# Optimization experiments

Measured on AMD Instinct MI355X. Metric: run time of the kernel, lower is better.

Reference implementation:

```python
import jax, jax.numpy as jnp
import numpy as np

NUM_HEADS = 8
LN_EPS = 1e-5


def layer_norm_chw(x, w, b):
    # LayerNorm over (C, H, W) jointly, elementwise affine of shape (C, H, W)
    mu = jnp.mean(x, axis=(1, 2, 3), keepdims=True)
    var = jnp.mean(jnp.square(x - mu), axis=(1, 2, 3), keepdims=True)
    return (x - mu) * jax.lax.rsqrt(var + LN_EPS) * w[None] + b[None]


def conv1x1(x, w, b):
    # 1x1 conv == per-pixel matmul. x: (B,C,H,W), w: (O,C), b: (O,)
    return jnp.einsum('bcxy,oc->boxy', x, w) + b[None, :, None, None]


def setup_inputs() -> dict:
    key = jax.random.key(0)
    ks = jax.random.split(key, 8)
    B, C, H, W = 16, 512, 64, 64
    Dq, Dv, Dh = 512, 512, 2048
    s = lambda fan_in: 1.0 / np.sqrt(fan_in)
    return {
        'x': jax.random.normal(ks[0], (B, C, H, W), jnp.float32),
        'ln1_w': jnp.ones((C, H, W), jnp.float32),
        'ln1_b': jnp.zeros((C, H, W), jnp.float32),
        'q_w': jax.random.normal(ks[1], (Dq, C), jnp.float32) * s(C),
        'q_b': jnp.zeros((Dq,), jnp.float32),
        'k_w': jax.random.normal(ks[2], (Dq, C), jnp.float32) * s(C),
        'k_b': jnp.zeros((Dq,), jnp.float32),
        'v_w': jax.random.normal(ks[3], (Dv, C), jnp.float32) * s(C),
        'v_b': jnp.zeros((Dv,), jnp.float32),
        'hu_w': jax.random.normal(ks[4], (C, Dv), jnp.float32) * s(Dv),
        'hu_b': jnp.zeros((C,), jnp.float32),
        'ln2_w': jnp.ones((C, H, W), jnp.float32),
        'ln2_b': jnp.zeros((C, H, W), jnp.float32),
        'ff1_w': jax.random.normal(ks[5], (Dh, C), jnp.float32) * s(C),
        'ff1_b': jnp.zeros((Dh,), jnp.float32),
        'ff2_w': jax.random.normal(ks[6], (C, Dh), jnp.float32) * s(Dh),
        'ff2_b': jnp.zeros((C,), jnp.float32),
    }


def reference(x, ln1_w, ln1_b, q_w, q_b, k_w, k_b, v_w, v_b,
              hu_w, hu_b, ln2_w, ln2_b, ff1_w, ff1_b, ff2_w, ff2_b):
    B, C, H, W = x.shape
    h = NUM_HEADS

    a = layer_norm_chw(x, ln1_w, ln1_b)
    Q = conv1x1(a, q_w, q_b)   # (B, Dq, H, W)
    K = conv1x1(a, k_w, k_b)   # (B, Dq, H, W)
    V = conv1x1(a, v_w, v_b)   # (B, Dv, H, W)

    Dq, Dv = Q.shape[1], V.shape[1]
    # softmax over channel dim for Q (per pixel, over all Dq channels)
    Q = jax.nn.softmax(Q, axis=1)
    # softmax over flattened spatial dim for K (per channel)
    K = jax.nn.softmax(K.reshape(B, Dq, H * W), axis=-1).reshape(B, Dq, H, W)

    # split heads: (B, h, d, H, W)
    Qh = Q.reshape(B, h, Dq // h, H, W)
    Kh = K.reshape(B, h, Dq // h, H, W)
    Vh = V.reshape(B, h, Dv // h, H, W)

    # linear attention: KV = sum_xy K ⊗ V, then per-pixel KV^T @ Q
    KV = jnp.einsum('bhkxy,bhvxy->bhkv', Kh, Vh)        # (B, h, dq, dv)
    attn = jnp.einsum('bhkv,bhkxy->bhvxy', KV, Qh)      # (B, h, dv, H, W)
    attn = attn.reshape(B, Dv, H, W)
    attn = conv1x1(attn, hu_w, hu_b)                    # (B, C, H, W)

    x = x + attn
    x = layer_norm_chw(x, ln2_w, ln2_b)
    ff = conv1x1(jax.nn.gelu(conv1x1(x, ff1_w, ff1_b), approximate=False), ff2_w, ff2_b)
    return x + ff
```

## Files before the change

### kernel.cpp

```cpp
#include <hip/hip_runtime.h>
#include <math.h>

#define BATCH 16
#define CCH   512
#define HWS   4096
#define CHW   (CCH*HWS)
#define DHFF  2048
#define NHEAD 8
#define HD    64
#define QKVLD 1536
#define LNEPS 1e-5f

typedef unsigned short u16;
typedef __bf16 bf16x8 __attribute__((ext_vector_type(8)));
typedef float f32x4 __attribute__((ext_vector_type(4)));

__device__ __forceinline__ float gelu_f(float x) {
    float y = 1.5957691216057308f * x * (1.0f + 0.044715f * x * x);
    return x / (1.0f + __expf(-y));
}
__device__ __forceinline__ u16 f2bf(float f) {
    union { float f; unsigned u; } c; c.f = f;
    unsigned r = c.u + 0x7FFFu + ((c.u >> 16) & 1u);
    return (u16)(r >> 16);
}
__device__ __forceinline__ float bf2f(u16 h) {
    union { unsigned u; float f; } c; c.u = ((unsigned)h) << 16; return c.f;
}
__device__ __forceinline__ uint2 pack_bf16x4(float v0, float v1, float v2, float v3) {
    union { uint2 u; __bf16 b[4]; } o;
    o.b[0] = (__bf16)v0; o.b[1] = (__bf16)v1; o.b[2] = (__bf16)v2; o.b[3] = (__bf16)v3;
    return o.u;
}
__device__ __forceinline__ void gld16(const u16* g, u16* l) {
    __builtin_amdgcn_global_load_lds((const __attribute__((address_space(1))) unsigned*)g,
                                     (__attribute__((address_space(3))) unsigned*)l, 16, 0, 0);
}

template<int K>
__device__ __forceinline__ void gemm_core(const u16* __restrict__ A,
                                          const u16* __restrict__ B,
                                          int m0, int n0,
                                          u16 (&As)[2][128 * 32],
                                          u16 (&Bs)[2][128 * 32],
                                          f32x4 (&acc)[4][4]) {
    const int tid = threadIdx.x;
    const int lane = tid & 63;
    const int w = tid >> 6;
    const int wm = (w & 1) * 64, wn = (w >> 1) * 64;
    const int ls = lane & 15, lq = lane >> 4;
#pragma unroll
    for (int i = 0; i < 4; ++i)
#pragma unroll
        for (int j = 0; j < 4; ++j) acc[i][j] = (f32x4){0.f, 0.f, 0.f, 0.f};

    const int srow = w * 16 + (lane >> 2);
    const int scol = (lane & 3) * 8;
    const u16* gA0 = A + (size_t)(m0 + srow) * K + scol;
    const u16* gA1 = gA0 + (size_t)64 * K;
    const u16* gB0 = B + (size_t)(n0 + srow) * K + scol;
    const u16* gB1 = gB0 + (size_t)64 * K;
    const int lo = w * 512;

    gld16(gA0, &As[0][lo]);
    gld16(gA1, &As[0][2048 + lo]);
    gld16(gB0, &Bs[0][lo]);
    gld16(gB1, &Bs[0][2048 + lo]);
    __syncthreads();

#pragma unroll 8
    for (int kt = 0; kt < K; kt += 32) {
        const int cur = (kt >> 5) & 1;
        const int nx = cur ^ 1;
        if (kt + 32 < K) {
            gld16(gA0 + kt + 32, &As[nx][lo]);
            gld16(gA1 + kt + 32, &As[nx][2048 + lo]);
            gld16(gB0 + kt + 32, &Bs[nx][lo]);
            gld16(gB1 + kt + 32, &Bs[nx][2048 + lo]);
        }
        bf16x8 af[4], bfv[4];
#pragma unroll
        for (int i = 0; i < 4; ++i)
            af[i] = *(bf16x8*)&As[cur][(wm + i * 16 + ls) * 32 + lq * 8];
#pragma unroll
        for (int j = 0; j < 4; ++j)
            bfv[j] = *(bf16x8*)&Bs[cur][(wn + j * 16 + ls) * 32 + lq * 8];
#pragma unroll
        for (int i = 0; i < 4; ++i)
#pragma unroll
            for (int j = 0; j < 4; ++j)
                acc[i][j] = __builtin_amdgcn_mfma_f32_16x16x32_bf16(bfv[j], af[i], acc[i][j], 0, 0, 0);
        if (kt + 32 < K)
            __syncthreads();
    }
}

__global__ __launch_bounds__(256) void stats_k(const float* __restrict__ src,
                                               float* __restrict__ st) {
    int b = blockIdx.y;
    const float4* p = (const float4*)(src + (size_t)b * CHW + (size_t)blockIdx.x * (CHW / 64));
    float s = 0.f, ss = 0.f;
    for (int i = threadIdx.x; i < (CHW / 64 / 4); i += 256) {
        float4 v = p[i];
        s  += v.x + v.y + v.z + v.w;
        ss += v.x * v.x + v.y * v.y + v.z * v.z + v.w * v.w;
    }
    __shared__ float r1[256], r2[256];
    int t = threadIdx.x;
    r1[t] = s; r2[t] = ss; __syncthreads();
    for (int o = 128; o > 0; o >>= 1) {
        if (t < o) { r1[t] += r1[t + o]; r2[t] += r2[t + o]; }
        __syncthreads();
    }
    if (t == 0) { atomicAdd(&st[2 * b], r1[0]); atomicAdd(&st[2 * b + 1], r2[0]); }
}

__global__ __launch_bounds__(256) void cvt_k(const float* __restrict__ src,
                                             u16* __restrict__ dst, int n4) {
    int i = blockIdx.x * 256 + threadIdx.x;
    if (i >= n4) return;
    float4 v = ((const float4*)src)[i];
    ((uint2*)dst)[i] = pack_bf16x4(v.x, v.y, v.z, v.w);
}

__global__ __launch_bounds__(256) void tr_k(const float* __restrict__ src,
                                            float* __restrict__ dst) {
    int p0 = blockIdx.x * 32, c0 = blockIdx.y * 32;
    __shared__ float T[32][33];
    int tx = threadIdx.x & 31, ty = threadIdx.x >> 5;
#pragma unroll
    for (int i = 0; i < 4; ++i)
        T[ty + i * 8][tx] = src[(size_t)(c0 + ty + i * 8) * HWS + p0 + tx];
    __syncthreads();
#pragma unroll
    for (int i = 0; i < 4; ++i)
        dst[(size_t)(p0 + ty + i * 8) * CCH + c0 + tx] = T[tx][ty + i * 8];
}

__global__ __launch_bounds__(256) void ln1t_k(const float* __restrict__ x,
                                              const float* __restrict__ w,
                                              const float* __restrict__ bb,
                                              const float* __restrict__ st,
                                              u16* __restrict__ a, int cb) {
    int p0 = blockIdx.x * 32, c0 = blockIdx.y * 32, bl = blockIdx.z;
    int b = cb + bl;
    float mean = st[2 * b] * (1.0f / CHW);
    float var  = st[2 * b + 1] * (1.0f / CHW) - mean * mean;
    float rstd = rsqrtf(var + LNEPS);
    __shared__ float T[32][33];
    int tx = threadIdx.x & 31, ty = threadIdx.x >> 5;
    const float* xb = x + (size_t)b * CHW;
#pragma unroll
    for (int i = 0; i < 4; ++i) {
        size_t o = (size_t)(c0 + ty + i * 8) * HWS + p0 + tx;
        T[ty + i * 8][tx] = (xb[o] - mean) * rstd * w[o] + bb[o];
    }
    __syncthreads();
    u16* ab = a + (size_t)bl * CHW;
#pragma unroll
    for (int i = 0; i < 4; ++i)
        ab[(size_t)(p0 + ty + i * 8) * CCH + c0 + tx] = f2bf(T[tx][ty + i * 8]);
}

template<int K, int ACT>
__global__ __launch_bounds__(256) void gemm_tn(const u16* __restrict__ A,
                                               const u16* __restrict__ B,
                                               const float* __restrict__ bias,
                                               u16* __restrict__ Out,
                                               int ldo, int nt) {
    __shared__ u16 As[2][128 * 32];
    __shared__ u16 Bs[2][128 * 32];
    const int cpx = gridDim.x >> 3;
    const int wg = ((int)blockIdx.x & 7) * cpx + ((int)blockIdx.x >> 3);
    const int m0 = (wg / nt) * 128;
    const int n0 = (wg % nt) * 128;
    f32x4 acc[4][4];
    gemm_core<K>(A, B, m0, n0, As, Bs, acc);

    const int lane = threadIdx.x & 63;
    const int w = threadIdx.x >> 6;
    const int wm = (w & 1) * 64, wn = (w >> 1) * 64;
    const int ls = lane & 15, lq = lane >> 4;
#pragma unroll
    for (int j = 0; j < 4; ++j) {
        int nb = n0 + wn + j * 16 + lq * 4;
        float4 bv = *(const float4*)&bias[nb];
#pragma unroll
        for (int i = 0; i < 4; ++i) {
            int m = m0 + wm + i * 16 + ls;
            float v0 = acc[i][j][0] + bv.x;
            float v1 = acc[i][j][1] + bv.y;
            float v2 = acc[i][j][2] + bv.z;
            float v3 = acc[i][j][3] + bv.w;
            if (ACT) { v0 = gelu_f(v0); v1 = gelu_f(v1); v2 = gelu_f(v2); v3 = gelu_f(v3); }
            *(uint2*)(Out + (size_t)m * ldo + nb) = pack_bf16x4(v0, v1, v2, v3);
        }
    }
}

__global__ __launch_bounds__(256) void gemm_hu_resid(const u16* __restrict__ A,
                                                     const u16* __restrict__ B,
                                                     const float* __restrict__ bias,
                                                     float* __restrict__ r,
                                                     const float* __restrict__ x,
                                                     float* __restrict__ pstat, int cb) {
    __shared__ u16 As[2][128 * 32];
    __shared__ u16 Bs[2][128 * 32];
    __shared__ float r1[256], r2[256];
    const int nt = 4;
    const int cpx = gridDim.x >> 3;
    const int wg = ((int)blockIdx.x & 7) * cpx + ((int)blockIdx.x >> 3);
    const int m0 = (wg / nt) * 128;
    const int n0 = (wg % nt) * 128;
    f32x4 acc[4][4];
    gemm_core<512>(A, B, m0, n0, As, Bs, acc);

    const int lane = threadIdx.x & 63;
    const int w = threadIdx.x >> 6;
    const int wm = (w & 1) * 64, wn = (w >> 1) * 64;
    const int ls = lane & 15, lq = lane >> 4;
    const int bl = m0 >> 12;
    const int p0loc = m0 & 4095;
    const float* xb = x + (size_t)(cb + bl) * CHW;
    float* rb = r + (size_t)bl * CHW;
    float s = 0.f, ss = 0.f;
#pragma unroll
    for (int j = 0; j < 4; ++j) {
        int nb = n0 + wn + j * 16 + lq * 4;
        float4 bv = *(const float4*)&bias[nb];
#pragma unroll
        for (int i = 0; i < 4; ++i) {
            int p = p0loc + wm + i * 16 + ls;
            float v0 = acc[i][j][0] + bv.x + xb[(size_t)(nb + 0) * HWS + p];
            float v1 = acc[i][j][1] + bv.y + xb[(size_t)(nb + 1) * HWS + p];
            float v2 = acc[i][j][2] + bv.z + xb[(size_t)(nb + 2) * HWS + p];
            float v3 = acc[i][j][3] + bv.w + xb[(size_t)(nb + 3) * HWS + p];
            *(float4*)(rb + (size_t)p * CCH + nb) = (float4){v0, v1, v2, v3};
            s  += v0 + v1 + v2 + v3;
            ss += v0 * v0 + v1 * v1 + v2 * v2 + v3 * v3;
        }
    }
    int t = threadIdx.x;
    __syncthreads();
    r1[t] = s; r2[t] = ss; __syncthreads();
    for (int o = 128; o > 0; o >>= 1) {
        if (t < o) { r1[t] += r1[t + o]; r2[t] += r2[t + o]; }
        __syncthreads();
    }
    if (t == 0) {
        int slot = ((p0loc >> 7) << 2) + (wg % nt);
        float* pp = pstat + ((size_t)(cb + bl) * 128 + slot) * 2;
        pp[0] = r1[0]; pp[1] = r2[0];
    }
}

__global__ __launch_bounds__(256) void gemm_ff2_final(const u16* __restrict__ A,
                                                      const u16* __restrict__ B,
                                                      const float* __restrict__ bias,
                                                      float* __restrict__ out,
                                                      const u16* __restrict__ x2,
                                                      int cb) {
    __shared__ union {
        struct { u16 As[2][128 * 32]; u16 Bs[2][128 * 32]; } g;
        float Tt[64][130];
    } shm;
    const int nt = 4;
    const int cpx = gridDim.x >> 3;
    const int wg = ((int)blockIdx.x & 7) * cpx + ((int)blockIdx.x >> 3);
    const int m0 = (wg / nt) * 128;
    const int n0 = (wg % nt) * 128;
    f32x4 acc[4][4];
    gemm_core<2048>(A, B, m0, n0, shm.g.As, shm.g.Bs, acc);

    const int tid = threadIdx.x;
    const int lane = tid & 63;
    const int w = tid >> 6;
    const int wm = (w & 1) * 64, wn = (w >> 1) * 64;
    const int ls = lane & 15, lq = lane >> 4;
    const int bl = m0 >> 12;
    const int p0loc = m0 & 4095;
    const u16* x2b = x2 + (size_t)bl * CHW;
    float* ob = out + (size_t)(cb + bl) * CHW;

    const int row = tid >> 2, mc = (tid & 3) * 32;
#pragma unroll
    for (int rnd = 0; rnd < 2; ++rnd) {
        __syncthreads();
        if ((wn >> 6) == rnd) {
#pragma unroll
            for (int j = 0; j < 4; ++j) {
                int nloc = wn + j * 16 + lq * 4;
                float4 bv = *(const float4*)&bias[n0 + nloc];
#pragma unroll
                for (int i = 0; i < 4; ++i) {
                    int m = wm + i * 16 + ls;
                    uint2 xr = *(const uint2*)&x2b[(size_t)(p0loc + m) * CCH + n0 + nloc];
                    u16* xp = (u16*)&xr;
                    int tr = nloc & 63;
                    shm.Tt[tr + 0][m] = acc[i][j][0] + bv.x + bf2f(xp[0]);
                    shm.Tt[tr + 1][m] = acc[i][j][1] + bv.y + bf2f(xp[1]);
                    shm.Tt[tr + 2][m] = acc[i][j][2] + bv.z + bf2f(xp[2]);
                    shm.Tt[tr + 3][m] = acc[i][j][3] + bv.w + bf2f(xp[3]);
                }
            }
        }
        __syncthreads();
        float* orow = ob + (size_t)(n0 + rnd * 64 + row) * HWS + p0loc + mc;
#pragma unroll
        for (int q = 0; q < 32; q += 4)
            *(float4*)(orow + q) = *(float4*)&shm.Tt[row][mc + q];
    }
}

__global__ __launch_bounds__(256) void softmax_row_k(u16* __restrict__ QKV) {
    int m = blockIdx.x * 4 + (threadIdx.x >> 6);
    int lane = threadIdx.x & 63;
    u16* row = QKV + (size_t)m * QKVLD + lane * 8;
    uint4 raw = *(uint4*)row;
    u16* pr = (u16*)&raw;
    float v[8];
#pragma unroll
    for (int i = 0; i < 8; ++i) v[i] = bf2f(pr[i]);
    float mx = v[0];
#pragma unroll
    for (int i = 1; i < 8; ++i) mx = fmaxf(mx, v[i]);
    for (int o = 32; o > 0; o >>= 1) mx = fmaxf(mx, __shfl_xor(mx, o, 64));
    float s = 0.f;
#pragma unroll
    for (int i = 0; i < 8; ++i) { v[i] = __expf(v[i] - mx); s += v[i]; }
    for (int o = 32; o > 0; o >>= 1) s += __shfl_xor(s, o, 64);
    float inv = 1.0f / s;
#pragma unroll
    for (int i = 0; i < 8; ++i) pr[i] = f2bf(v[i] * inv);
    *(uint4*)row = raw;
}

__global__ __launch_bounds__(256) void kcolstat_k(const u16* __restrict__ QKV,
                                                  float* __restrict__ kpart) {
    int pc = blockIdx.x, bl = blockIdx.y;
    int cg = threadIdx.x & 63;
    int ps = threadIdx.x >> 6;
    const u16* base = QKV + (size_t)bl * HWS * QKVLD + CCH + cg * 8;
    int p0 = pc * 256 + ps * 64;
    float m[8];
#pragma unroll
    for (int i = 0; i < 8; ++i) m[i] = -1e30f;
    for (int p = p0; p < p0 + 64; ++p) {
        uint4 r = *(const uint4*)(base + (size_t)p * QKVLD);
        u16* rp = (u16*)&r;
#pragma unroll
        for (int i = 0; i < 8; ++i) m[i] = fmaxf(m[i], bf2f(rp[i]));
    }
    __shared__ float red[4][512];
#pragma unroll
    for (int i = 0; i < 8; ++i) red[ps][cg * 8 + i] = m[i];
    __syncthreads();
#pragma unroll
    for (int i = 0; i < 8; ++i)
        m[i] = fmaxf(fmaxf(red[0][cg * 8 + i], red[1][cg * 8 + i]),
                     fmaxf(red[2][cg * 8 + i], red[3][cg * 8 + i]));
    __syncthreads();
    float s[8];
#pragma unroll
    for (int i = 0; i < 8; ++i) s[i] = 0.f;
    for (int p = p0; p < p0 + 64; ++p) {
        uint4 r = *(const uint4*)(base + (size_t)p * QKVLD);
        u16* rp = (u16*)&r;
#pragma unroll
        for (int i = 0; i < 8; ++i) s[i] += __expf(bf2f(rp[i]) - m[i]);
    }
#pragma unroll
    for (int i = 0; i < 8; ++i) red[ps][cg * 8 + i] = s[i];
    __syncthreads();
    if (ps == 0) {
        float* outp = kpart + (((size_t)bl * 16 + pc) * 512 + cg * 8) * 2;
#pragma unroll
        for (int i = 0; i < 8; ++i) {
            float sv = red[0][cg * 8 + i] + red[1][cg * 8 + i] +
                       red[2][cg * 8 + i] + red[3][cg * 8 + i];
            outp[2 * i] = m[i]; outp[2 * i + 1] = sv;
        }
    }
}

__global__ __launch_bounds__(256) void kcolmerge_k(const float* __restrict__ kpart,
                                                   float* __restrict__ kstat) {
    int bl = blockIdx.x;
#pragma unroll
    for (int j = 0; j < 2; ++j) {
        int col = threadIdx.x * 2 + j;
        float m = -1e30f;
        for (int pc = 0; pc < 16; ++pc)
            m = fmaxf(m, kpart[(((size_t)bl * 16 + pc) * 512 + col) * 2]);
        float s = 0.f;
        for (int pc = 0; pc < 16; ++pc) {
            const float* p = kpart + (((size_t)bl * 16 + pc) * 512 + col) * 2;
            s += p[1] * __expf(p[0] - m);
        }
        kstat[((size_t)bl * 512 + col) * 2]     = m;
        kstat[((size_t)bl * 512 + col) * 2 + 1] = 1.0f / s;
    }
}

__global__ __launch_bounds__(256) void kv_k2(const u16* __restrict__ QKV,
                                             const float* __restrict__ kstat,
                                             float* __restrict__ KV) {
    int pc = blockIdx.x, h = blockIdx.y, bl = blockIdx.z;
    const u16* kbase = QKV + (size_t)bl * HWS * QKVLD + CCH + h * HD;
    const u16* vbase = kbase + CCH;
    float* kvb = KV + ((size_t)bl * NHEAD + h) * (HD * HD);
    __shared__ float Ks[64][65], Vs[64][65];
    __shared__ float Ms[64], Is[64];
    int tid = threadIdx.x;
    if (tid < 64) {
        const float* sp = kstat + ((size_t)bl * 512 + h * HD + tid) * 2;
        Ms[tid] = sp[0]; Is[tid] = sp[1];
    }
    int tk = tid >> 4, tv = tid & 15;
    float acc[4][4];
#pragma unroll
    for (int i = 0; i < 4; ++i)
#pragma unroll
        for (int j = 0; j < 4; ++j) acc[i][j] = 0.f;

    for (int s = 0; s < 4; ++s) {
        int pbase = pc * 256 + s * 64;
        __syncthreads();
#pragma unroll
        for (int j = 0; j < 2; ++j) {
            int li = tid + j * 256;
            int pl = li >> 3, c8 = (li & 7) * 8;
            uint4 kr = *(const uint4*)(kbase + (size_t)(pbase + pl) * QKVLD + c8);
            uint4 vr = *(const uint4*)(vbase + (size_t)(pbase + pl) * QKVLD + c8);
            u16* kp = (u16*)&kr; u16* vp = (u16*)&vr;
#pragma unroll
            for (int t = 0; t < 8; ++t) {
                Ks[pl][c8 + t] = __expf(bf2f(kp[t]) - Ms[c8 + t]) * Is[c8 + t];
                Vs[pl][c8 + t] = bf2f(vp[t]);
            }
        }
        __syncthreads();
#pragma unroll 4
        for (int p = 0; p < 64; ++p) {
            float ka[4], va[4];
#pragma unroll
            for (int i = 0; i < 4; ++i) { ka[i] = Ks[p][tk * 4 + i]; va[i] = Vs[p][tv * 4 + i]; }
#pragma unroll
            for (int i = 0; i < 4; ++i)
#pragma unroll
                for (int j = 0; j < 4; ++j) acc[i][j] += ka[i] * va[j];
        }
    }
#pragma unroll
    for (int i = 0; i < 4; ++i)
#pragma unroll
        for (int j = 0; j < 4; ++j)
            atomicAdd(&kvb[(size_t)(tk * 4 + i) * HD + tv * 4 + j], acc[i][j]);
}

__global__ __launch_bounds__(256) void attn_k2(const u16* __restrict__ QKV,
                                               const float* __restrict__ KV,
                                               u16* __restrict__ attnRaw) {
    int pt = blockIdx.x, h = blockIdx.y, bl = blockIdx.z;
    const u16* qbase = QKV + (size_t)bl * HWS * QKVLD + h * HD;
    const float* kvb = KV + ((size_t)bl * NHEAD + h) * (HD * HD);
    __shared__ float KVs[64][68], Qs[64][68];
    int tid = threadIdx.x;
#pragma unroll
    for (int j = 0; j < 4; ++j) {
        int li = tid + j * 256;
        int k = li >> 4, c4 = (li & 15) * 4;
        *(float4*)&KVs[k][c4] = *(const float4*)(kvb + (size_t)k * HD + c4);
    }
#pragma unroll
    for (int j = 0; j < 2; ++j) {
        int li = tid + j * 256;
        int pl = li >> 3, c8 = (li & 7) * 8;
        uint4 qr = *(const uint4*)(qbase + (size_t)(pt * 64 + pl) * QKVLD + c8);
        u16* qp = (u16*)&qr;
#pragma unroll
        for (int t = 0; t < 8; ++t) Qs[pl][c8 + t] = bf2f(qp[t]);
    }
    __syncthreads();
    int tp = tid >> 4, tv = tid & 15;
    float acc[4][4];
#pragma unroll
    for (int i = 0; i < 4; ++i)
#pragma unroll
        for (int j = 0; j < 4; ++j) acc[i][j] = 0.f;
#pragma unroll 4
    for (int k = 0; k < 64; ++k) {
        float qa[4], kv4[4];
#pragma unroll
        for (int i = 0; i < 4; ++i) { qa[i] = Qs[tp * 4 + i][k]; kv4[i] = KVs[k][tv * 4 + i]; }
#pragma unroll
        for (int i = 0; i < 4; ++i)
#pragma unroll
            for (int j = 0; j < 4; ++j) acc[i][j] += qa[i] * kv4[j];
    }
#pragma unroll
    for (int i = 0; i < 4; ++i) {
        *(uint2*)(attnRaw + (size_t)(bl * HWS + pt * 64 + tp * 4 + i) * CCH + h * HD + tv * 4) =
            pack_bf16x4(acc[i][0], acc[i][1], acc[i][2], acc[i][3]);
    }
}

__global__ __launch_bounds__(128) void red2_k(const float* __restrict__ pstat,
                                              float* __restrict__ st, int cb) {
    int b = cb + blockIdx.x;
    const float* p = pstat + (size_t)b * 256;
    int t = threadIdx.x;
    float s = p[2 * t], ss = p[2 * t + 1];
    for (int o = 32; o > 0; o >>= 1) { s += __shfl_down(s, o, 64); ss += __shfl_down(ss, o, 64); }
    __shared__ float sh[4];
    if ((t & 63) == 0) { sh[(t >> 6) * 2] = s; sh[(t >> 6) * 2 + 1] = ss; }
    __syncthreads();
    if (t == 0) { st[32 + 2 * b] = sh[0] + sh[2]; st[32 + 2 * b + 1] = sh[1] + sh[3]; }
}

__global__ __launch_bounds__(256) void ln2a_k(const float* __restrict__ r,
                                              const float* __restrict__ w2t,
                                              const float* __restrict__ b2t,
                                              const float* __restrict__ st,
                                              u16* __restrict__ x2, int cb) {
    size_t i4 = (size_t)blockIdx.x * 256 + threadIdx.x;
    int bl = (int)(i4 / (CHW / 4));
    int b = cb + bl;
    size_t off4 = i4 % (CHW / 4);
    float mean = st[32 + 2 * b] * (1.0f / CHW);
    float var  = st[32 + 2 * b + 1] * (1.0f / CHW) - mean * mean;
    float rstd = rsqrtf(var + LNEPS);
    float4 v  = ((const float4*)(r + (size_t)bl * CHW))[off4];
    float4 wv = ((const float4*)w2t)[off4];
    float4 bv = ((const float4*)b2t)[off4];
    ((uint2*)(x2 + (size_t)bl * CHW))[off4] =
        pack_bf16x4((v.x - mean) * rstd * wv.x + bv.x,
                    (v.y - mean) * rstd * wv.y + bv.y,
                    (v.z - mean) * rstd * wv.z + bv.z,
                    (v.w - mean) * rstd * wv.w + bv.w);
}

extern "C" void kernel_launch(void* const* d_in, const int* in_sizes, int n_in,
                              void* d_out, int out_size, void* d_ws, size_t ws_size,
                              hipStream_t stream) {
    const float* x    = (const float*)d_in[0];
    const float* ln1w = (const float*)d_in[1];
    const float* ln1b = (const float*)d_in[2];
    const float* qw   = (const float*)d_in[3];
    const float* qb   = (const float*)d_in[4];
    const float* kw   = (const float*)d_in[5];
    const float* kb   = (const float*)d_in[6];
    const float* vw   = (const float*)d_in[7];
    const float* vb   = (const float*)d_in[8];
    const float* huw  = (const float*)d_in[9];
    const float* hub  = (const float*)d_in[10];
    const float* ln2w = (const float*)d_in[11];
    const float* ln2b = (const float*)d_in[12];
    const float* f1w  = (const float*)d_in[13];
    const float* f1b  = (const float*)d_in[14];
    const float* f2w  = (const float*)d_in[15];
    const float* f2b  = (const float*)d_in[16];
    float* out = (float*)d_out;
    float* ws = (float*)d_ws;

    float* stats = ws;
    float* qkvb  = ws + 64;
    u16*   wqkv  = (u16*)(ws + 1600);
    u16*   whu   = (u16*)(ws + 394816);
    u16*   wf1   = (u16*)(ws + 525888);
    u16*   wf2   = (u16*)(ws + 1050176);
    float* w2t   = ws + 1574464;
    float* b2t   = ws + 3671616;
    float* pstat = ws + 5768768;
    float* kpart = ws + 5834304;
    float* kstat = ws + 6096448;
    float* kvbuf = ws + 6112832;

    int G = 16;
    while (G > 1 && (6112832ull + (size_t)G * 5275648ull) * 4ull > ws_size) G >>= 1;
    const int nch = BATCH / G;
    const size_t U = (size_t)G * CHW;

    float* R       = kvbuf + (size_t)G * 32768;
    u16*   a_bf    = (u16*)R;
    u16*   QKVb    = (u16*)(R + U / 2);
    float* rbuf    = R + 3 * U / 2;
    u16*   x2bf    = (u16*)R;
    u16*   Hbuf    = (u16*)(R + U / 2);

    hipMemsetAsync(stats, 0, 64 * sizeof(float), stream);

    cvt_k<<<dim3(256), 256, 0, stream>>>(qw, wqkv, 65536);
    cvt_k<<<dim3(256), 256, 0, stream>>>(kw, wqkv + 262144, 65536);
    cvt_k<<<dim3(256), 256, 0, stream>>>(vw, wqkv + 524288, 65536);
    cvt_k<<<dim3(256), 256, 0, stream>>>(huw, whu, 65536);
    cvt_k<<<dim3(1024), 256, 0, stream>>>(f1w, wf1, 262144);
    cvt_k<<<dim3(1024), 256, 0, stream>>>(f2w, wf2, 262144);
    tr_k<<<dim3(128, 16), 256, 0, stream>>>(ln2w, w2t);
    tr_k<<<dim3(128, 16), 256, 0, stream>>>(ln2b, b2t);
    hipMemcpyAsync(qkvb,        qb, 512 * sizeof(float), hipMemcpyDeviceToDevice, stream);
    hipMemcpyAsync(qkvb + 512,  kb, 512 * sizeof(float), hipMemcpyDeviceToDevice, stream);
    hipMemcpyAsync(qkvb + 1024, vb, 512 * sizeof(float), hipMemcpyDeviceToDevice, stream);

    stats_k<<<dim3(64, BATCH), 256, 0, stream>>>(x, stats);

    for (int g = 0; g < nch; ++g) {
        const int cb = g * G;
        const int mt = G * 32;
        ln1t_k<<<dim3(128, 16, G), 256, 0, stream>>>(x, ln1w, ln1b, stats, a_bf, cb);
        gemm_tn<512, 0><<<dim3(mt * 12), 256, 0, stream>>>(a_bf, wqkv, qkvb, QKVb, QKVLD, 12);
        softmax_row_k<<<dim3(G * 1024), 256, 0, stream>>>(QKVb);
        kcolstat_k<<<dim3(16, G), 256, 0, stream>>>(QKVb, kpart);
        kcolmerge_k<<<dim3(G), 256, 0, stream>>>(kpart, kstat);
        hipMemsetAsync(kvbuf, 0, (size_t)G * 32768 * sizeof(float), stream);
        kv_k2<<<dim3(16, NHEAD, G), 256, 0, stream>>>(QKVb, kstat, kvbuf);
        attn_k2<<<dim3(64, NHEAD, G), 256, 0, stream>>>(QKVb, kvbuf, a_bf);
        gemm_hu_resid<<<dim3(mt * 4), 256, 0, stream>>>(a_bf, whu, hub, rbuf, x, pstat, cb);
        red2_k<<<dim3(G), 128, 0, stream>>>(pstat, stats, cb);
        ln2a_k<<<dim3(G * 2048), 256, 0, stream>>>(rbuf, w2t, b2t, stats, x2bf, cb);
        gemm_tn<512, 1><<<dim3(mt * 16), 256, 0, stream>>>(x2bf, wf1, f1b, Hbuf, DHFF, 16);
        gemm_ff2_final<<<dim3(mt * 4), 256, 0, stream>>>(Hbuf, wf2, f2b, out, x2bf, cb);
    }
}
```

Measured before the change: 1.451 ms.

## Deepen GEMM K-tile to 64 with XOR-swizzled LDS layout

```diff
diff --git a/kernel.cpp b/kernel.cpp
--- a/kernel.cpp
+++ b/kernel.cpp
@@ -41,8 +41,8 @@
 __device__ __forceinline__ void gemm_core(const u16* __restrict__ A,
                                           const u16* __restrict__ B,
                                           int m0, int n0,
-                                          u16 (&As)[2][128 * 32],
-                                          u16 (&Bs)[2][128 * 32],
+                                          u16 (&As)[2][8192],
+                                          u16 (&Bs)[2][8192],
                                           f32x4 (&acc)[4][4]) {
     const int tid = threadIdx.x;
     const int lane = tid & 63;
@@ -54,43 +54,49 @@
 #pragma unroll
         for (int j = 0; j < 4; ++j) acc[i][j] = (f32x4){0.f, 0.f, 0.f, 0.f};
 
-    const int srow = w * 16 + (lane >> 2);
-    const int scol = (lane & 3) * 8;
-    const u16* gA0 = A + (size_t)(m0 + srow) * K + scol;
-    const u16* gA1 = gA0 + (size_t)64 * K;
-    const u16* gB0 = B + (size_t)(n0 + srow) * K + scol;
-    const u16* gB1 = gB0 + (size_t)64 * K;
-    const int lo = w * 512;
-
-    gld16(gA0, &As[0][lo]);
-    gld16(gA1, &As[0][2048 + lo]);
-    gld16(gB0, &Bs[0][lo]);
-    gld16(gB1, &Bs[0][2048 + lo]);
+    const int sr = w * 16 + (lane >> 3);
+    const int sc = ((lane & 7) ^ (lane >> 3)) * 8;
+    const u16* gA0 = A + (size_t)(m0 + sr) * K + sc;
+    const u16* gB0 = B + (size_t)(n0 + sr) * K + sc;
+    const int lo = w * 1024;
+
+    auto STG = [&](int buf, int kt) {
+        gld16(gA0 + kt,                    &As[buf][lo]);
+        gld16(gA0 + kt + (size_t)8 * K,    &As[buf][lo + 512]);
+        gld16(gA0 + kt + (size_t)64 * K,   &As[buf][lo + 4096]);
+        gld16(gA0 + kt + (size_t)72 * K,   &As[buf][lo + 4608]);
+        gld16(gB0 + kt,                    &Bs[buf][lo]);
+        gld16(gB0 + kt + (size_t)8 * K,    &Bs[buf][lo + 512]);
+        gld16(gB0 + kt + (size_t)64 * K,   &Bs[buf][lo + 4096]);
+        gld16(gB0 + kt + (size_t)72 * K,   &Bs[buf][lo + 4608]);
+    };
+
+    STG(0, 0);
     __syncthreads();
 
 #pragma unroll 8
-    for (int kt = 0; kt < K; kt += 32) {
-        const int cur = (kt >> 5) & 1;
-        const int nx = cur ^ 1;
-        if (kt + 32 < K) {
-            gld16(gA0 + kt + 32, &As[nx][lo]);
-            gld16(gA1 + kt + 32, &As[nx][2048 + lo]);
-            gld16(gB0 + kt + 32, &Bs[nx][lo]);
-            gld16(gB1 + kt + 32, &Bs[nx][2048 + lo]);
-        }
-        bf16x8 af[4], bfv[4];
-#pragma unroll
-        for (int i = 0; i < 4; ++i)
-            af[i] = *(bf16x8*)&As[cur][(wm + i * 16 + ls) * 32 + lq * 8];
-#pragma unroll
-        for (int j = 0; j < 4; ++j)
-            bfv[j] = *(bf16x8*)&Bs[cur][(wn + j * 16 + ls) * 32 + lq * 8];
-#pragma unroll
-        for (int i = 0; i < 4; ++i)
+    for (int kt = 0; kt < K; kt += 64) {
+        const int cur = (kt >> 6) & 1;
+        if (kt + 64 < K)
+            STG(cur ^ 1, kt + 64);
+#pragma unroll
+        for (int kk = 0; kk < 2; ++kk) {
+            bf16x8 af[4], bfv[4];
+#pragma unroll
+            for (int i = 0; i < 4; ++i)
+                af[i] = *(bf16x8*)&As[cur][(wm + i * 16 + ls) * 64 +
+                                           (((kk * 4 + lq) ^ (ls & 7)) * 8)];
 #pragma unroll
             for (int j = 0; j < 4; ++j)
-                acc[i][j] = __builtin_amdgcn_mfma_f32_16x16x32_bf16(bfv[j], af[i], acc[i][j], 0, 0, 0);
-        if (kt + 32 < K)
+                bfv[j] = *(bf16x8*)&Bs[cur][(wn + j * 16 + ls) * 64 +
+                                            (((kk * 4 + lq) ^ (ls & 7)) * 8)];
+#pragma unroll
+            for (int i = 0; i < 4; ++i)
+#pragma unroll
+                for (int j = 0; j < 4; ++j)
+                    acc[i][j] = __builtin_amdgcn_mfma_f32_16x16x32_bf16(bfv[j], af[i], acc[i][j], 0, 0, 0);
+        }
+        if (kt + 64 < K)
             __syncthreads();
     }
 }
@@ -168,8 +174,8 @@
                                                const float* __restrict__ bias,
                                                u16* __restrict__ Out,
                                                int ldo, int nt) {
-    __shared__ u16 As[2][128 * 32];
-    __shared__ u16 Bs[2][128 * 32];
+    __shared__ u16 As[2][8192];
+    __shared__ u16 Bs[2][8192];
     const int cpx = gridDim.x >> 3;
     const int wg = ((int)blockIdx.x & 7) * cpx + ((int)blockIdx.x >> 3);
     const int m0 = (wg / nt) * 128;
@@ -204,16 +210,17 @@
                                                      float* __restrict__ r,
                                                      const float* __restrict__ x,
                                                      float* __restrict__ pstat, int cb) {
-    __shared__ u16 As[2][128 * 32];
-    __shared__ u16 Bs[2][128 * 32];
-    __shared__ float r1[256], r2[256];
+    __shared__ union {
+        struct { u16 As[2][8192]; u16 Bs[2][8192]; } g;
+        struct { float r1[256]; float r2[256]; } red;
+    } shm;
     const int nt = 4;
     const int cpx = gridDim.x >> 3;
     const int wg = ((int)blockIdx.x & 7) * cpx + ((int)blockIdx.x >> 3);
     const int m0 = (wg / nt) * 128;
     const int n0 = (wg % nt) * 128;
     f32x4 acc[4][4];
-    gemm_core<512>(A, B, m0, n0, As, Bs, acc);
+    gemm_core<512>(A, B, m0, n0, shm.g.As, shm.g.Bs, acc);
 
     const int lane = threadIdx.x & 63;
     const int w = threadIdx.x >> 6;
@@ -242,15 +249,15 @@
     }
     int t = threadIdx.x;
     __syncthreads();
-    r1[t] = s; r2[t] = ss; __syncthreads();
+    shm.red.r1[t] = s; shm.red.r2[t] = ss; __syncthreads();
     for (int o = 128; o > 0; o >>= 1) {
-        if (t < o) { r1[t] += r1[t + o]; r2[t] += r2[t + o]; }
+        if (t < o) { shm.red.r1[t] += shm.red.r1[t + o]; shm.red.r2[t] += shm.red.r2[t + o]; }
         __syncthreads();
     }
     if (t == 0) {
         int slot = ((p0loc >> 7) << 2) + (wg % nt);
         float* pp = pstat + ((size_t)(cb + bl) * 128 + slot) * 2;
-        pp[0] = r1[0]; pp[1] = r2[0];
+        pp[0] = shm.red.r1[0]; pp[1] = shm.red.r2[0];
     }
 }
 
@@ -261,7 +268,7 @@
                                                       const u16* __restrict__ x2,
                                                       int cb) {
     __shared__ union {
-        struct { u16 As[2][128 * 32]; u16 Bs[2][128 * 32]; } g;
+        struct { u16 As[2][8192]; u16 Bs[2][8192]; } g;
         float Tt[64][130];
     } shm;
     const int nt = 4;
```

New measurement: 1.387 ms. -4.4%, faster.
